# Optimization experiments

Measured on AMD Instinct MI355X. Metric: run time of the kernel, lower is better.

Reference implementation:

```python
import jax, jax.numpy as jnp
import numpy as np

IN_CH = 32
OUT_CH = 32
B, N = 1, 100000
E = 1600000
BN_EPS = 1e-5


def setup_inputs() -> dict:
    key = jax.random.key(0)
    k1, k2, k3 = jax.random.split(key, 3)
    x = jax.random.normal(k1, (B, IN_CH, N, 1), dtype=jnp.float32)
    edge_index = jax.random.randint(k2, (2, E), 0, B * N, dtype=jnp.int64)
    # Conv1d(in*2 -> out, kernel_size=1, bias=False): weight [out, 2*in]
    W = jax.random.normal(k3, (OUT_CH, 2 * IN_CH), dtype=jnp.float32) * (1.0 / np.sqrt(2 * IN_CH))
    gamma = jnp.ones((OUT_CH,), dtype=jnp.float32)
    beta = jnp.zeros((OUT_CH,), dtype=jnp.float32)
    return {"x": x, "edge_index": edge_index, "W": W, "gamma": gamma, "beta": beta}


def reference(x, edge_index, W, gamma, beta):
    Bb, C, Nn, _ = x.shape
    out_ch = W.shape[0]
    # faithful to torch: x.squeeze(-1).view(B*N, C) (raw row-major reshape)
    x_flat = x[..., 0].reshape(Bb * Nn, C)
    src, tgt = edge_index[0], edge_index[1]
    x_s = x_flat[src]                      # [E, C] gather
    x_t = x_flat[tgt]                      # [E, C] gather
    ef = jnp.concatenate([x_s, x_t - x_s], axis=1)  # [E, 2C]
    y = ef @ W.T                           # 1x1 conv == GEMM, [E, out]
    # BatchNorm1d in training mode: batch stats over edge dim (biased var)
    mean = jnp.mean(y, axis=0)
    var = jnp.mean(jnp.square(y - mean), axis=0)
    y = (y - mean) * jax.lax.rsqrt(var + BN_EPS) * gamma + beta
    # ELU (alpha=1)
    y = jnp.where(y > 0, y, jnp.expm1(y))
    out = jnp.zeros((Bb * Nn, out_ch), dtype=y.dtype).at[src].add(y)  # scatter-add
    return out.reshape(Bb, out_ch, Nn)[..., None]
```

## Files before the change

kernel.cpp:

```cpp
#include <hip/hip_runtime.h>
#include <hip/hip_bf16.h>
#include <math.h>

#define NCH 32

typedef unsigned short ushort_t;
typedef unsigned int uint_t;

static __device__ __forceinline__ float bf2f(ushort_t b) {
    return __uint_as_float(((uint_t)b) << 16);
}
static __device__ __forceinline__ ushort_t f2bf(float f) {
    __hip_bfloat16 h = __float2bfloat16(f);
    return *reinterpret_cast<ushort_t*>(&h);
}


__global__ __launch_bounds__(256) void k_uv2(
    const float* __restrict__ x, const float* __restrict__ W,
    float* __restrict__ u, ushort_t* __restrict__ vh, int N)
{
    __shared__ float At[NCH * NCH];
    __shared__ float Bt[NCH * NCH];
    for (int i = threadIdx.x; i < NCH * NCH; i += 256) {
        const int k = i >> 5, c = i & 31;
        const float w1 = W[c * 64 + k];
        const float w2 = W[c * 64 + 32 + k];
        At[i] = w1 - w2;
        Bt[i] = w2;
    }
    __syncthreads();

    const int n = blockIdx.x * 8 + (threadIdx.x >> 5);
    const int c = threadIdx.x & 31;
    if (n >= N) return;

    const float xc = x[(size_t)n * NCH + c];
    float su = 0.f, sv = 0.f;
#pragma unroll
    for (int k = 0; k < NCH; ++k) {
        const float xk = __shfl(xc, k, 32);
        su = fmaf(At[k * 32 + c], xk, su);
        sv = fmaf(Bt[k * 32 + c], xk, sv);
    }
    u[(size_t)n * NCH + c] = su;
    vh[(size_t)n * NCH + c] = f2bf(sv);
}

__global__ __launch_bounds__(256) void k_stats_flat(
    const float* __restrict__ u, const ushort_t* __restrict__ vh,
    const int* __restrict__ srci, const int* __restrict__ tgti,
    int* __restrict__ cnt_n,
    float* __restrict__ partials, int E)
{
    float sum[NCH], ssq[NCH];
#pragma unroll
    for (int c = 0; c < NCH; ++c) { sum[c] = 0.f; ssq[c] = 0.f; }

    const int stride = gridDim.x * 256;
    for (int e = blockIdx.x * 256 + threadIdx.x; e < E; e += stride) {
        const int s = srci[e];
        const int t = tgti[e];
        atomicAdd(&cnt_n[s], 1);
        const float4* __restrict__ pu = (const float4*)(u + (size_t)s * NCH);
        const uint_t* __restrict__ pw = (const uint_t*)(vh + (size_t)t * NCH);
        float us[NCH];
#pragma unroll
        for (int i = 0; i < 8; ++i) {
            float4 a = pu[i];
            us[4*i+0] = a.x; us[4*i+1] = a.y; us[4*i+2] = a.z; us[4*i+3] = a.w;
        }
#pragma unroll
        for (int k = 0; k < 16; ++k) {
            uint_t w2 = pw[k];
            float v0 = __uint_as_float((w2 & 0xFFFFu) << 16);
            float v1 = __uint_as_float(w2 & 0xFFFF0000u);
            const int c0 = 2*k, c1 = 2*k + 1;
            float y0 = us[c0] + v0;
            float y1 = us[c1] + v1;
            sum[c0] += y0; ssq[c0] = fmaf(y0, y0, ssq[c0]);
            sum[c1] += y1; ssq[c1] = fmaf(y1, y1, ssq[c1]);
        }
    }

#pragma unroll
    for (int c = 0; c < NCH; ++c) {
#pragma unroll
        for (int off = 32; off > 0; off >>= 1) {
            sum[c] += __shfl_down(sum[c], off);
            ssq[c] += __shfl_down(ssq[c], off);
        }
    }
    __shared__ float red[4][64];
    const int lane = threadIdx.x & 63, wave = threadIdx.x >> 6;
    if (lane == 0) {
#pragma unroll
        for (int c = 0; c < NCH; ++c) { red[wave][c] = sum[c]; red[wave][NCH+c] = ssq[c]; }
    }
    __syncthreads();
    if (threadIdx.x < 64)
        partials[(size_t)blockIdx.x * 64 + threadIdx.x] =
            red[0][threadIdx.x] + red[1][threadIdx.x]
          + red[2][threadIdx.x] + red[3][threadIdx.x];
}

__global__ __launch_bounds__(256) void k_scan1(
    const int* __restrict__ counts,
    int* __restrict__ offsets,
    int* __restrict__ blksum,
    int N)
{
    const int tid = threadIdx.x;
    const int base = blockIdx.x * 1024 + tid * 4;
    int c0 = 0, c1 = 0, c2 = 0, c3 = 0;
    if (base + 3 < N) {
        const int4 q = *(const int4*)(counts + base);
        c0 = q.x; c1 = q.y; c2 = q.z; c3 = q.w;
    } else {
        if (base + 0 < N) c0 = counts[base + 0];
        if (base + 1 < N) c1 = counts[base + 1];
        if (base + 2 < N) c2 = counts[base + 2];
        if (base + 3 < N) c3 = counts[base + 3];
    }
    const int tsum = c0 + c1 + c2 + c3;

    const int lane = tid & 63, wv = tid >> 6;
    int val = tsum;
#pragma unroll
    for (int off = 1; off < 64; off <<= 1) {
        int t = __shfl_up(val, off);
        if (lane >= off) val += t;
    }
    __shared__ int wsum[4];
    __shared__ int woff[4];
    if (lane == 63) wsum[wv] = val;
    __syncthreads();
    if (tid == 0) {
        int a = 0;
#pragma unroll
        for (int w = 0; w < 4; ++w) { woff[w] = a; a += wsum[w]; }
        blksum[blockIdx.x] = a;
    }
    __syncthreads();
    int run = woff[wv] + (val - tsum);
    if (base + 0 < N) { offsets[base + 0] = run; run += c0; }
    if (base + 1 < N) { offsets[base + 1] = run; run += c1; }
    if (base + 2 < N) { offsets[base + 2] = run; run += c2; }
    if (base + 3 < N) { offsets[base + 3] = run; }
}

__global__ __launch_bounds__(1024) void k_scan2(int* __restrict__ blksum, int NBLK)
{
    const int tid = threadIdx.x;
    int v = (tid < NBLK) ? blksum[tid] : 0;
    const int lane = tid & 63, wv = tid >> 6;
    int val = v;
#pragma unroll
    for (int off = 1; off < 64; off <<= 1) {
        int t = __shfl_up(val, off);
        if (lane >= off) val += t;
    }
    __shared__ int wsum[16];
    __shared__ int woff[16];
    if (lane == 63) wsum[wv] = val;
    __syncthreads();
    if (tid == 0) {
        int a = 0;
#pragma unroll
        for (int w = 0; w < 16; ++w) { woff[w] = a; a += wsum[w]; }
    }
    __syncthreads();
    if (tid < NBLK) blksum[tid] = woff[wv] + val - v;
}

__global__ __launch_bounds__(256) void k_scan3(
    int* __restrict__ offsets, int* __restrict__ cursor,
    const int* __restrict__ blksum, int N)
{
    const int i = blockIdx.x * 256 + threadIdx.x;
    if (i >= N) return;
    const int o = offsets[i] + blksum[i >> 10];
    offsets[i] = o;
    cursor[i]  = o;
}

__global__ __launch_bounds__(256) void k_tperm_part(
    const int* __restrict__ srci, const int* __restrict__ tgti,
    int* __restrict__ cur_n, int* __restrict__ tperm,
    int E, uint_t magic)
{
    const int team   = blockIdx.x & 7;
    const int trank  = blockIdx.x >> 3;
    const int tcount = gridDim.x >> 3;
    const int stride = tcount * 256;
    for (int e = trank * 256 + threadIdx.x; e < E; e += stride) {
        const int s = srci[e];
        int part = (int)__umulhi((uint_t)s, magic);
        part = min(part, 7);
        if (part != team) continue;
        const int pos = atomicAdd(&cur_n[s], 1);
        tperm[pos] = tgti[e];
    }
}

__global__ __launch_bounds__(256) void k_finalize(
    const float* __restrict__ partials, int nblocks,
    const float* __restrict__ gamma, const float* __restrict__ beta,
    float* __restrict__ ab, float invE)
{
    __shared__ float acc[4][64];
    const int vtx = threadIdx.x & 63, chunk = threadIdx.x >> 6;
    float s = 0.f;
    for (int r = chunk; r < nblocks; r += 4) s += partials[(size_t)r * 64 + vtx];
    acc[chunk][vtx] = s;
    __syncthreads();
    if (threadIdx.x < 64) acc[0][vtx] = acc[0][vtx] + acc[1][vtx] + acc[2][vtx] + acc[3][vtx];
    __syncthreads();
    if (threadIdx.x < 32) {
        const int c = threadIdx.x;
        float mean = acc[0][c] * invE;
        float var  = acc[0][32 + c] * invE - mean * mean;
        float rstd = rsqrtf(var + 1e-5f);
        float a = gamma[c] * rstd;
        ab[c] = a; ab[32 + c] = beta[c] - mean * a;
    }
}

__global__ __launch_bounds__(256) void k_apply_node(
    const float* __restrict__ u, const ushort_t* __restrict__ vh,
    const int* __restrict__ tperm, const int* __restrict__ off_n,
    const int* __restrict__ cnt_n, const float* __restrict__ ab,
    float* __restrict__ out, int N)
{
    const int n = blockIdx.x * 8 + (threadIdx.x >> 5);
    const int c = threadIdx.x & 31;
    if (n >= N) return;

    const int off = off_n[n];
    const int deg = cnt_n[n];
    const float un  = u[(size_t)n * NCH + c];
    const float a_c = ab[c];
    const float b_c = ab[32 + c];

    float acc = 0.f;
    int i = 0;
    for (; i + 4 <= deg; i += 4) {
        int t0 = tperm[off + i + 0];
        int t1 = tperm[off + i + 1];
        int t2 = tperm[off + i + 2];
        int t3 = tperm[off + i + 3];
        ushort_t v0 = vh[(size_t)t0 * NCH + c];
        ushort_t v1 = vh[(size_t)t1 * NCH + c];
        ushort_t v2 = vh[(size_t)t2 * NCH + c];
        ushort_t v3 = vh[(size_t)t3 * NCH + c];
        float z0 = fmaf(a_c, un + bf2f(v0), b_c);
        float z1 = fmaf(a_c, un + bf2f(v1), b_c);
        float z2 = fmaf(a_c, un + bf2f(v2), b_c);
        float z3 = fmaf(a_c, un + bf2f(v3), b_c);
        z0 = (z0 > 0.f) ? z0 : (__expf(z0) - 1.0f);
        z1 = (z1 > 0.f) ? z1 : (__expf(z1) - 1.0f);
        z2 = (z2 > 0.f) ? z2 : (__expf(z2) - 1.0f);
        z3 = (z3 > 0.f) ? z3 : (__expf(z3) - 1.0f);
        acc += (z0 + z1) + (z2 + z3);
    }
    for (; i < deg; ++i) {
        int t = tperm[off + i];
        float z = fmaf(a_c, un + bf2f(vh[(size_t)t * NCH + c]), b_c);
        z = (z > 0.f) ? z : (__expf(z) - 1.0f);
        acc += z;
    }
    out[(size_t)n * NCH + c] = acc;
}

__global__ __launch_bounds__(256) void k_stats_hist(
    const float* __restrict__ x,
    const int* __restrict__ srci, const int* __restrict__ tgti,
    const float* __restrict__ W,
    float* __restrict__ partials, int E)
{
    float sum[NCH], ssq[NCH];
#pragma unroll
    for (int c = 0; c < NCH; ++c) { sum[c] = 0.f; ssq[c] = 0.f; }
    const int stride = gridDim.x * blockDim.x;
    for (int e = blockIdx.x * blockDim.x + threadIdx.x; e < E; e += stride) {
        const int s = srci[e], t = tgti[e];
        const float4* ps = (const float4*)(x + (size_t)s * NCH);
        const float4* pt = (const float4*)(x + (size_t)t * NCH);
        float xs[NCH], dx[NCH];
#pragma unroll
        for (int i = 0; i < 8; ++i) {
            float4 a = ps[i], bb = pt[i];
            xs[4*i+0] = a.x; xs[4*i+1] = a.y; xs[4*i+2] = a.z; xs[4*i+3] = a.w;
            dx[4*i+0] = bb.x - a.x; dx[4*i+1] = bb.y - a.y;
            dx[4*i+2] = bb.z - a.z; dx[4*i+3] = bb.w - a.w;
        }
#pragma unroll
        for (int c = 0; c < NCH; ++c) {
            const float* wr = W + c * 64;
            float y = 0.f;
#pragma unroll
            for (int k = 0; k < NCH; ++k) y = fmaf(wr[k], xs[k], y);
#pragma unroll
            for (int k = 0; k < NCH; ++k) y = fmaf(wr[32 + k], dx[k], y);
            sum[c] += y;
            ssq[c] = fmaf(y, y, ssq[c]);
        }
    }
#pragma unroll
    for (int c = 0; c < NCH; ++c) {
#pragma unroll
        for (int off = 32; off > 0; off >>= 1) {
            sum[c] += __shfl_down(sum[c], off);
            ssq[c] += __shfl_down(ssq[c], off);
        }
    }
    __shared__ float red[4][64];
    const int lane = threadIdx.x & 63, wave = threadIdx.x >> 6;
    if (lane == 0) {
#pragma unroll
        for (int c = 0; c < NCH; ++c) { red[wave][c] = sum[c]; red[wave][NCH+c] = ssq[c]; }
    }
    __syncthreads();
    if (threadIdx.x < 64)
        partials[(size_t)blockIdx.x * 64 + threadIdx.x] =
            red[0][threadIdx.x] + red[1][threadIdx.x] + red[2][threadIdx.x] + red[3][threadIdx.x];
}

__global__ __launch_bounds__(256) void k_apply_atomic(
    const float* __restrict__ x,
    const int* __restrict__ srci, const int* __restrict__ tgti,
    const float* __restrict__ W, const float* __restrict__ ab,
    float* __restrict__ out, int E)
{
    const int e = blockIdx.x * 256 + threadIdx.x;
    if (e >= E) return;
    const int s = srci[e], t = tgti[e];
    const float4* ps = (const float4*)(x + (size_t)s * NCH);
    const float4* pt = (const float4*)(x + (size_t)t * NCH);
    float xs[NCH], dx[NCH];
#pragma unroll
    for (int i = 0; i < 8; ++i) {
        float4 a = ps[i], bb = pt[i];
        xs[4*i+0] = a.x; xs[4*i+1] = a.y; xs[4*i+2] = a.z; xs[4*i+3] = a.w;
        dx[4*i+0] = bb.x - a.x; dx[4*i+1] = bb.y - a.y;
        dx[4*i+2] = bb.z - a.z; dx[4*i+3] = bb.w - a.w;
    }
    float* orow = out + (size_t)s * NCH;
#pragma unroll
    for (int c = 0; c < NCH; ++c) {
        const float* wr = W + c * 64;
        float y = 0.f;
#pragma unroll
        for (int k = 0; k < NCH; ++k) y = fmaf(wr[k], xs[k], y);
#pragma unroll
        for (int k = 0; k < NCH; ++k) y = fmaf(wr[32 + k], dx[k], y);
        float z = fmaf(ab[c], y, ab[32 + c]);
        z = (z > 0.f) ? z : (__expf(z) - 1.0f);
        atomicAdd(orow + c, z);
    }
}

extern "C" void kernel_launch(void* const* d_in, const int* in_sizes, int n_in,
                              void* d_out, int out_size, void* d_ws, size_t ws_size,
                              hipStream_t stream)
{
    const float* x     = (const float*)d_in[0];
    const int*   ei    = (const int*)d_in[1];
    const float* W     = (const float*)d_in[2];
    const float* gamma = (const float*)d_in[3];
    const float* beta  = (const float*)d_in[4];
    const int E = in_sizes[1] / 2;
    const int N = in_sizes[0] / NCH;
    const int* srci = ei;
    const int* tgti = ei + E;

    const int SB = 512;
    const int NBLK = (N + 1023) / 1024;

    const uint_t partDiv = (uint_t)((N + 7) / 8);
    const uint_t magic = (uint_t)((0x100000000ULL + partDiv - 1) / partDiv);

    size_t need = (size_t)N * NCH * 4 + (size_t)N * NCH * 2
                + ((size_t)E + 3 * (size_t)N + 1024) * 4
                + ((size_t)SB * 64 + 64) * 4;

    if (NBLK <= 1024 && ws_size >= need) {
        float*    u       = (float*)d_ws;
        ushort_t* vh      = (ushort_t*)(u + (size_t)N * NCH);
        int*      tperm   = (int*)(vh + (size_t)N * NCH);
        int*      cnt_n   = tperm + E;
        int*      off_n   = cnt_n + N;
        int*      cur_n   = off_n + N;
        int*      blksum  = cur_n + N;
        float*    partials= (float*)(blksum + 1024);
        float*    ab      = partials + (size_t)SB * 64;

        hipMemsetAsync(cnt_n, 0, (size_t)N * sizeof(int), stream);
        k_uv2<<<(N + 7) / 8, 256, 0, stream>>>(x, W, u, vh, N);
        k_stats_flat<<<SB, 256, 0, stream>>>(u, vh, srci, tgti, cnt_n, partials, E);
        k_scan1<<<NBLK, 256, 0, stream>>>(cnt_n, off_n, blksum, N);
        k_scan2<<<1, 1024, 0, stream>>>(blksum, NBLK);
        k_scan3<<<(N + 255) / 256, 256, 0, stream>>>(off_n, cur_n, blksum, N);
        k_tperm_part<<<512, 256, 0, stream>>>(srci, tgti, cur_n, tperm, E, magic);
        k_finalize<<<1, 256, 0, stream>>>(partials, SB, gamma, beta, ab, 1.0f / (float)E);
        k_apply_node<<<(N + 7) / 8, 256, 0, stream>>>(u, vh, tperm, off_n, cnt_n, ab,
                                                      (float*)d_out, N);
    } else {
        const int SBf = 512;
        float* ab       = (float*)d_ws;
        float* partials = ab + 64;
        hipMemsetAsync(d_out, 0, (size_t)out_size * sizeof(float), stream);
        k_stats_hist<<<SBf, 256, 0, stream>>>(x, srci, tgti, W, partials, E);
        k_finalize<<<1, 256, 0, stream>>>(partials, SBf, gamma, beta, ab, 1.0f / (float)E);
        k_apply_atomic<<<(E + 255) / 256, 256, 0, stream>>>(x, srci, tgti, W, ab,
                                                            (float*)d_out, E);
    }
}
```

Baseline: 361.0 us.

## Store u in bf16 and build CSR via two-level bucket sort

The per-node u projection is now stored as bf16 rather than fp32, which halves the bytes gathered in the stats and apply kernels. The single-pass partitioned atomic scatter into per-node cursors is replaced by a two-level binning. First, edges are appended to 64-node buckets with one global atomic per edge, packing the local node id and the target into one int. Then one block per bucket does a shared-memory histogram and scatter to produce tperm. This cuts global atomic contention and the 8x redundant edge scans, at the cost of an extra payload buffer, a bf16 rounding error on u, and a limit of 17 bits (about 131k nodes) for the packed target index.

```diff
diff --git a/kernel.cpp b/kernel.cpp
--- a/kernel.cpp
+++ b/kernel.cpp
@@ -16,9 +16,9 @@
 }
 
 
-__global__ __launch_bounds__(256) void k_uv2(
+__global__ __launch_bounds__(256) void k_uv2b(
     const float* __restrict__ x, const float* __restrict__ W,
-    float* __restrict__ u, ushort_t* __restrict__ vh, int N)
+    ushort_t* __restrict__ uh, ushort_t* __restrict__ vh, int N)
 {
     __shared__ float At[NCH * NCH];
     __shared__ float Bt[NCH * NCH];
@@ -43,12 +43,12 @@
         su = fmaf(At[k * 32 + c], xk, su);
         sv = fmaf(Bt[k * 32 + c], xk, sv);
     }
-    u[(size_t)n * NCH + c] = su;
+    uh[(size_t)n * NCH + c] = f2bf(su);
     vh[(size_t)n * NCH + c] = f2bf(sv);
 }
 
 __global__ __launch_bounds__(256) void k_stats_flat(
-    const float* __restrict__ u, const ushort_t* __restrict__ vh,
+    const ushort_t* __restrict__ uh, const ushort_t* __restrict__ vh,
     const int* __restrict__ srci, const int* __restrict__ tgti,
     int* __restrict__ cnt_n,
     float* __restrict__ partials, int E)
@@ -62,22 +62,23 @@
         const int s = srci[e];
         const int t = tgti[e];
         atomicAdd(&cnt_n[s], 1);
-        const float4* __restrict__ pu = (const float4*)(u + (size_t)s * NCH);
+        const uint_t* __restrict__ pu = (const uint_t*)(uh + (size_t)s * NCH);
         const uint_t* __restrict__ pw = (const uint_t*)(vh + (size_t)t * NCH);
-        float us[NCH];
-#pragma unroll
-        for (int i = 0; i < 8; ++i) {
-            float4 a = pu[i];
-            us[4*i+0] = a.x; us[4*i+1] = a.y; us[4*i+2] = a.z; us[4*i+3] = a.w;
-        }
+        uint_t ub[16], wb[16];
+#pragma unroll
+        for (int k = 0; k < 16; ++k) ub[k] = pu[k];
+#pragma unroll
+        for (int k = 0; k < 16; ++k) wb[k] = pw[k];
 #pragma unroll
         for (int k = 0; k < 16; ++k) {
-            uint_t w2 = pw[k];
-            float v0 = __uint_as_float((w2 & 0xFFFFu) << 16);
-            float v1 = __uint_as_float(w2 & 0xFFFF0000u);
+            const uint_t a2 = ub[k], w2 = wb[k];
+            const float u0 = __uint_as_float((a2 & 0xFFFFu) << 16);
+            const float u1 = __uint_as_float(a2 & 0xFFFF0000u);
+            const float v0 = __uint_as_float((w2 & 0xFFFFu) << 16);
+            const float v1 = __uint_as_float(w2 & 0xFFFF0000u);
             const int c0 = 2*k, c1 = 2*k + 1;
-            float y0 = us[c0] + v0;
-            float y1 = us[c1] + v1;
+            const float y0 = u0 + v0;
+            const float y1 = u1 + v1;
             sum[c0] += y0; ssq[c0] = fmaf(y0, y0, ssq[c0]);
             sum[c1] += y1; ssq[c1] = fmaf(y1, y1, ssq[c1]);
         }
@@ -174,32 +175,59 @@
 }
 
 __global__ __launch_bounds__(256) void k_scan3(
-    int* __restrict__ offsets, int* __restrict__ cursor,
+    int* __restrict__ offsets, int* __restrict__ cur_b,
     const int* __restrict__ blksum, int N)
 {
     const int i = blockIdx.x * 256 + threadIdx.x;
     if (i >= N) return;
     const int o = offsets[i] + blksum[i >> 10];
     offsets[i] = o;
-    cursor[i]  = o;
-}
-
-__global__ __launch_bounds__(256) void k_tperm_part(
+    if ((i & 63) == 0) cur_b[i >> 6] = o;
+}
+
+__global__ __launch_bounds__(256) void k_binA(
     const int* __restrict__ srci, const int* __restrict__ tgti,
-    int* __restrict__ cur_n, int* __restrict__ tperm,
-    int E, uint_t magic)
-{
-    const int team   = blockIdx.x & 7;
-    const int trank  = blockIdx.x >> 3;
-    const int tcount = gridDim.x >> 3;
-    const int stride = tcount * 256;
-    for (int e = trank * 256 + threadIdx.x; e < E; e += stride) {
-        const int s = srci[e];
-        int part = (int)__umulhi((uint_t)s, magic);
-        part = min(part, 7);
-        if (part != team) continue;
-        const int pos = atomicAdd(&cur_n[s], 1);
-        tperm[pos] = tgti[e];
+    int* __restrict__ cur_b, int* __restrict__ payload, int E)
+{
+    const int e = blockIdx.x * 256 + threadIdx.x;
+    if (e >= E) return;
+    const int s = srci[e];
+    const int pos = atomicAdd(&cur_b[s >> 6], 1);
+    payload[pos] = ((s & 63) << 17) | tgti[e];
+}
+
+__global__ __launch_bounds__(256) void k_binB(
+    const int* __restrict__ payload, const int* __restrict__ off_n,
+    int* __restrict__ tperm, int N, int E)
+{
+    __shared__ int h[64];
+    __shared__ int cur[64];
+    const int b = blockIdx.x;
+    const int boff = off_n[b << 6];
+    const int nxt = (b + 1) << 6;
+    const int bend = (nxt < N) ? off_n[nxt] : E;
+    const int bcnt = bend - boff;
+
+    if (threadIdx.x < 64) h[threadIdx.x] = 0;
+    __syncthreads();
+    for (int i = threadIdx.x; i < bcnt; i += 256)
+        atomicAdd(&h[(payload[boff + i] >> 17) & 63], 1);
+    __syncthreads();
+    if (threadIdx.x < 64) {
+        const int v = h[threadIdx.x];
+        int val = v;
+#pragma unroll
+        for (int off = 1; off < 64; off <<= 1) {
+            int t = __shfl_up(val, off);
+            if (threadIdx.x >= (uint_t)off) val += t;
+        }
+        cur[threadIdx.x] = boff + (val - v);
+    }
+    __syncthreads();
+    for (int i = threadIdx.x; i < bcnt; i += 256) {
+        const int w = payload[boff + i];
+        const int pos = atomicAdd(&cur[(w >> 17) & 63], 1);
+        tperm[pos] = w & 0x1FFFF;
     }
 }
 
@@ -227,7 +255,7 @@
 }
 
 __global__ __launch_bounds__(256) void k_apply_node(
-    const float* __restrict__ u, const ushort_t* __restrict__ vh,
+    const ushort_t* __restrict__ uh, const ushort_t* __restrict__ vh,
     const int* __restrict__ tperm, const int* __restrict__ off_n,
     const int* __restrict__ cnt_n, const float* __restrict__ ab,
     float* __restrict__ out, int N)
@@ -238,7 +266,7 @@
 
     const int off = off_n[n];
     const int deg = cnt_n[n];
-    const float un  = u[(size_t)n * NCH + c];
+    const float un  = bf2f(uh[(size_t)n * NCH + c]);
     const float a_c = ab[c];
     const float b_c = ab[32 + c];
 
@@ -376,34 +404,34 @@
 
     const int SB = 512;
     const int NBLK = (N + 1023) / 1024;
-
-    const uint_t partDiv = (uint_t)((N + 7) / 8);
-    const uint_t magic = (uint_t)((0x100000000ULL + partDiv - 1) / partDiv);
-
-    size_t need = (size_t)N * NCH * 4 + (size_t)N * NCH * 2
-                + ((size_t)E + 3 * (size_t)N + 1024) * 4
+    const int NB = (N + 63) >> 6;
+
+    size_t need = (size_t)N * NCH * 2 * 2
+                + ((size_t)E * 2 + 2 * (size_t)N + (size_t)NB + 1024) * 4
                 + ((size_t)SB * 64 + 64) * 4;
 
     if (NBLK <= 1024 && ws_size >= need) {
-        float*    u       = (float*)d_ws;
-        ushort_t* vh      = (ushort_t*)(u + (size_t)N * NCH);
+        ushort_t* uh      = (ushort_t*)d_ws;
+        ushort_t* vh      = uh + (size_t)N * NCH;
         int*      tperm   = (int*)(vh + (size_t)N * NCH);
-        int*      cnt_n   = tperm + E;
+        int*      payload = tperm + E;
+        int*      cnt_n   = payload + E;
         int*      off_n   = cnt_n + N;
-        int*      cur_n   = off_n + N;
-        int*      blksum  = cur_n + N;
+        int*      cur_b   = off_n + N;
+        int*      blksum  = cur_b + NB;
         float*    partials= (float*)(blksum + 1024);
         float*    ab      = partials + (size_t)SB * 64;
 
         hipMemsetAsync(cnt_n, 0, (size_t)N * sizeof(int), stream);
-        k_uv2<<<(N + 7) / 8, 256, 0, stream>>>(x, W, u, vh, N);
-        k_stats_flat<<<SB, 256, 0, stream>>>(u, vh, srci, tgti, cnt_n, partials, E);
+        k_uv2b<<<(N + 7) / 8, 256, 0, stream>>>(x, W, uh, vh, N);
+        k_stats_flat<<<SB, 256, 0, stream>>>(uh, vh, srci, tgti, cnt_n, partials, E);
         k_scan1<<<NBLK, 256, 0, stream>>>(cnt_n, off_n, blksum, N);
         k_scan2<<<1, 1024, 0, stream>>>(blksum, NBLK);
-        k_scan3<<<(N + 255) / 256, 256, 0, stream>>>(off_n, cur_n, blksum, N);
-        k_tperm_part<<<512, 256, 0, stream>>>(srci, tgti, cur_n, tperm, E, magic);
+        k_scan3<<<(N + 255) / 256, 256, 0, stream>>>(off_n, cur_b, blksum, N);
+        k_binA<<<(E + 255) / 256, 256, 0, stream>>>(srci, tgti, cur_b, payload, E);
+        k_binB<<<NB, 256, 0, stream>>>(payload, off_n, tperm, N, E);
         k_finalize<<<1, 256, 0, stream>>>(partials, SB, gamma, beta, ab, 1.0f / (float)E);
-        k_apply_node<<<(N + 7) / 8, 256, 0, stream>>>(u, vh, tperm, off_n, cnt_n, ab,
+        k_apply_node<<<(N + 7) / 8, 256, 0, stream>>>(uh, vh, tperm, off_n, cnt_n, ab,
                                                       (float*)d_out, N);
     } else {
         const int SBf = 512;
```

Measured after the change: 529.3 us. 1.47x slower.
